# Kernel tuning notes

Measured on AMD Instinct MI355X. Metric: run time of the kernel, lower is better.

## Reference

```python
import jax, jax.numpy as jnp
import numpy as np

B, T, D, H = 2, 2048, 1024, 16

def setup_inputs() -> dict:
    key = jax.random.key(0)
    k0, k1, k2, k3 = jax.random.split(key, 4)
    s = 0.02
    return {
        "x": jax.random.normal(k0, (B, T, D), dtype=jnp.float32),
        "Wqkv": jax.random.normal(k1, (3 * D, D), dtype=jnp.float32) * s,
        "Wout": jax.random.normal(k2, (D, D), dtype=jnp.float32) * s,
        "bout": jax.random.normal(k3, (D,), dtype=jnp.float32) * s,
    }

def reference(x, Wqkv, Wout, bout):
    b, t, d = x.shape
    h = H
    dh = d // h
    qkv = x @ Wqkv.T  # [b,t,3d]
    q, k, v = jnp.split(qkv, 3, axis=-1)
    def merge_heads(z):
        return z.reshape(b, t, h, dh).transpose(0, 2, 1, 3)  # [b,h,t,dh]
    q, k, v = map(merge_heads, (q, k, v))
    scale = dh ** -0.5
    dots = jnp.einsum('bhid,bhjd->bhij', q, k) * scale  # [b,h,t,t]
    causal_mask = jnp.triu(jnp.ones((t, t), dtype=bool), 1)
    dots = jnp.where(causal_mask, -jnp.inf, dots)
    attn = jax.nn.softmax(dots, axis=-1)
    out = jnp.einsum('bhij,bhjd->bhid', attn, v)  # [b,h,t,dh]
    out = out.transpose(0, 2, 1, 3).reshape(b, t, d)
    return out @ Wout.T + bout
```

## Files before the change

kernel.cpp:

```cpp
#include <hip/hip_runtime.h>
#include <hip/hip_bf16.h>
#include <math.h>

typedef __bf16 bf16x8 __attribute__((ext_vector_type(8)));
typedef float f32x4 __attribute__((ext_vector_type(4)));
typedef unsigned short u16;
typedef unsigned int u32;

#define EXP2F(x) __builtin_amdgcn_exp2f(x)

constexpr int Bz = 2, T = 2048, D = 1024, H = 16;
constexpr int M = Bz * T;
constexpr int NQKV = 3 * D;
constexpr float SCALE2 = 0.125f * 1.44269504089f;

#define GLD_LDS16(g, l) __builtin_amdgcn_global_load_lds( \
    (__attribute__((address_space(1))) void*)(g),          \
    (__attribute__((address_space(3))) void*)(l), 16, 0, 0)

__global__ void f32_to_bf16_kernel(const float* __restrict__ in,
                                   u16* __restrict__ out, int n4) {
  int i = blockIdx.x * blockDim.x + threadIdx.x;
  int stride = gridDim.x * blockDim.x;
  for (; i < n4; i += stride) {
    float4 f = ((const float4*)in)[i];
    ushort4 u;
    u.x = __builtin_bit_cast(u16, (__bf16)f.x);
    u.y = __builtin_bit_cast(u16, (__bf16)f.y);
    u.z = __builtin_bit_cast(u16, (__bf16)f.z);
    u.w = __builtin_bit_cast(u16, (__bf16)f.w);
    ((ushort4*)out)[i] = u;
  }
}

template <bool FP32OUT, bool QSCALE>
__global__ __launch_bounds__(256, 2)
void gemm_bt(const u16* __restrict__ A, const u16* __restrict__ Bm,
             u16* __restrict__ outb, float* __restrict__ outf,
             const float* __restrict__ bias, int K, int ldc) {
  __shared__ __align__(16) u16 sA[128 * 64];
  __shared__ __align__(16) u16 sB[128 * 64];
  const int tid = threadIdx.x;
  const int lane = tid & 63;
  const int wid = tid >> 6;
  const int wr = wid >> 1, wc = wid & 1;

  const int nwg = gridDim.x * gridDim.y;
  const int flat = blockIdx.y * gridDim.x + blockIdx.x;
  const int cpx = nwg >> 3;
  const int swz = (flat & 7) * cpx + (flat >> 3);
  const int bx = swz % gridDim.x;
  const int by = swz / gridDim.x;

  const int row0 = by * 128;
  const int col0 = bx * 128;

  f32x4 acc[4][4];
#pragma unroll
  for (int m = 0; m < 4; ++m)
#pragma unroll
    for (int n = 0; n < 4; ++n) acc[m][n] = (f32x4){0.f, 0.f, 0.f, 0.f};

  const int nk = K >> 6;
  for (int kt = 0; kt < nk; ++kt) {
    const int k0 = kt << 6;
#pragma unroll
    for (int i = 0; i < 4; ++i) {
      int off = i * 4096 + tid * 16;
      int r = off >> 7;
      int cs = (off >> 4) & 7;
      int c = cs ^ (r & 7);
      const u16* ga = A + (size_t)(row0 + r) * K + k0 + c * 8;
      const u16* gb = Bm + (size_t)(col0 + r) * K + k0 + c * 8;
      u16* la = sA + (i * 4096 + (tid & ~63) * 16) / 2;
      u16* lb = sB + (i * 4096 + (tid & ~63) * 16) / 2;
      GLD_LDS16(ga, la);
      GLD_LDS16(gb, lb);
    }
    __syncthreads();
#pragma unroll
    for (int kk = 0; kk < 2; ++kk) {
      bf16x8 af[4], bfv[4];
#pragma unroll
      for (int m = 0; m < 4; ++m) {
        int r = wr * 64 + m * 16 + (lane & 15);
        int cs = (kk * 4 + (lane >> 4)) ^ (r & 7);
        af[m] = *(const bf16x8*)(sA + r * 64 + cs * 8);
      }
#pragma unroll
      for (int n = 0; n < 4; ++n) {
        int r = wc * 64 + n * 16 + (lane & 15);
        int cs = (kk * 4 + (lane >> 4)) ^ (r & 7);
        bfv[n] = *(const bf16x8*)(sB + r * 64 + cs * 8);
      }
#pragma unroll
      for (int m = 0; m < 4; ++m)
#pragma unroll
        for (int n = 0; n < 4; ++n)
          acc[m][n] = __builtin_amdgcn_mfma_f32_16x16x32_bf16(
              af[m], bfv[n], acc[m][n], 0, 0, 0);
    }
    __syncthreads();
  }

  const int orow0 = row0 + wr * 64;
  const int ocol0 = col0 + wc * 64;
#pragma unroll
  for (int m = 0; m < 4; ++m)
#pragma unroll
    for (int n = 0; n < 4; ++n)
#pragma unroll
      for (int j = 0; j < 4; ++j) {
        int rr = orow0 + m * 16 + (lane >> 4) * 4 + j;
        int cc = ocol0 + n * 16 + (lane & 15);
        if (FP32OUT) {
          outf[(size_t)rr * ldc + cc] = acc[m][n][j] + bias[cc];
        } else {
          float v = acc[m][n][j];
          if (QSCALE && cc < D) v *= SCALE2;
          outb[(size_t)rr * ldc + cc] = __builtin_bit_cast(u16, (__bf16)v);
        }
      }
}

__global__ __launch_bounds__(256, 3)
void flash_kernel(const u16* __restrict__ qkv, u16* __restrict__ attn_out) {
  __shared__ __align__(16) u16 sK[2][64 * 64];
  __shared__ __align__(16) u16 sVt[2][64 * 72];
  __shared__ __align__(16) u16 sP[4][16][72];

  const int tid = threadIdx.x;
  const int lane = tid & 63;
  const int l15 = lane & 15;
  const int hi = lane >> 4;
  const int w = tid >> 6;
  const int bh = blockIdx.x;
  const int b = bh >> 4, h = bh & 15;
  const int qt = (gridDim.y - 1) - blockIdx.y;
  const int q0 = qt * 64;
  const int nv = qt + 1;

  const size_t base = (size_t)b * T * 3072;
  const u16* qp = qkv + base + 0 * 1024 + h * 64;
  const u16* kp = qkv + base + 1 * 1024 + h * 64;
  const u16* vp = qkv + base + 2 * 1024 + h * 64;

  ushort4 vr[2][2];
  auto stageK = [&](u16* dst, int kt) {
#pragma unroll
    for (int i = 0; i < 2; ++i) {
      int off = i * 4096 + tid * 16;
      int r = off >> 7;
      int cs = (off >> 4) & 7;
      int c = cs ^ (r & 7);
      GLD_LDS16(kp + (size_t)(kt * 64 + r) * 3072 + c * 8,
                dst + (i * 4096 + (tid & ~63) * 16) / 2);
    }
  };
  auto loadV = [&](int kt) {
#pragma unroll
    for (int i = 0; i < 2; ++i) {
      const u16* gsrc = vp + (size_t)(kt * 64 + lane) * 3072 + (i * 4 + w) * 8;
      vr[i][0] = ((const ushort4*)gsrc)[0];
      vr[i][1] = ((const ushort4*)gsrc)[1];
    }
  };
  auto writeV = [&](u16* dst) {
#pragma unroll
    for (int i = 0; i < 2; ++i) {
      int c = i * 4 + w;
      dst[(c * 8 + 0) * 72 + lane] = vr[i][0].x;
      dst[(c * 8 + 1) * 72 + lane] = vr[i][0].y;
      dst[(c * 8 + 2) * 72 + lane] = vr[i][0].z;
      dst[(c * 8 + 3) * 72 + lane] = vr[i][0].w;
      dst[(c * 8 + 4) * 72 + lane] = vr[i][1].x;
      dst[(c * 8 + 5) * 72 + lane] = vr[i][1].y;
      dst[(c * 8 + 6) * 72 + lane] = vr[i][1].z;
      dst[(c * 8 + 7) * 72 + lane] = vr[i][1].w;
    }
  };

  bf16x8 qf[2];
#pragma unroll
  for (int kk = 0; kk < 2; ++kk)
    qf[kk] = *(const bf16x8*)(qp + (size_t)(q0 + w * 16 + l15) * 3072 +
                              kk * 32 + hi * 8);

  f32x4 o_acc[4];
#pragma unroll
  for (int n = 0; n < 4; ++n) o_acc[n] = (f32x4){0.f, 0.f, 0.f, 0.f};
  float m2 = -INFINITY, l_run = 0.f;

  stageK(sK[0], 0);
  loadV(0);
  writeV(sVt[0]);
  __syncthreads();

  for (int v = 0; v < nv; ++v) {
    const int cur = v & 1;
    const int k0 = v * 64;
    if (v + 1 < nv) {
      stageK(sK[cur ^ 1], v + 1);
      loadV(v + 1);
    }

    bf16x8 kf[2][4];
#pragma unroll
    for (int kk = 0; kk < 2; ++kk)
#pragma unroll
      for (int n = 0; n < 4; ++n) {
        int rk = n * 16 + l15;
        int cs = (kk * 4 + hi) ^ (rk & 7);
        kf[kk][n] = *(const bf16x8*)(&sK[cur][rk * 64 + cs * 8]);
      }

    f32x4 sc[4];
#pragma unroll
    for (int n = 0; n < 4; ++n) sc[n] = (f32x4){0.f, 0.f, 0.f, 0.f};
#pragma unroll
    for (int kk = 0; kk < 2; ++kk)
#pragma unroll
      for (int n = 0; n < 4; ++n)
        sc[n] = __builtin_amdgcn_mfma_f32_16x16x32_bf16(kf[kk][n], qf[kk],
                                                        sc[n], 0, 0, 0);

    const bool diag = (v == nv - 1);
    const int qrow = q0 + w * 16 + l15;
    float mx = -INFINITY;
#pragma unroll
    for (int n = 0; n < 4; ++n)
#pragma unroll
      for (int r = 0; r < 4; ++r) {
        float sv = sc[n][r];
        if (diag) {
          int kpos = k0 + n * 16 + hi * 4 + r;
          if (kpos > qrow) sv = -INFINITY;
        }
        sc[n][r] = sv;
        mx = fmaxf(mx, sv);
      }
    mx = fmaxf(mx, __shfl_xor(mx, 16, 64));
    mx = fmaxf(mx, __shfl_xor(mx, 32, 64));

    const bool skip = __all(mx <= m2);
    float alpha = 1.f;
    if (!skip) {
      float mn = fmaxf(m2, mx);
      alpha = EXP2F(m2 - mn);
      m2 = mn;
    }

    float sum = 0.f;
#pragma unroll
    for (int n = 0; n < 4; ++n) {
      float p0 = EXP2F(sc[n][0] - m2);
      float p1 = EXP2F(sc[n][1] - m2);
      float p2 = EXP2F(sc[n][2] - m2);
      float p3 = EXP2F(sc[n][3] - m2);
      sum += (p0 + p1) + (p2 + p3);
      u32 w01 = ((u32)__builtin_bit_cast(u16, (__bf16)p1) << 16) |
                __builtin_bit_cast(u16, (__bf16)p0);
      u32 w23 = ((u32)__builtin_bit_cast(u16, (__bf16)p3) << 16) |
                __builtin_bit_cast(u16, (__bf16)p2);
      *(u32*)(&sP[w][l15][n * 16 + hi * 4 + 0]) = w01;
      *(u32*)(&sP[w][l15][n * 16 + hi * 4 + 2]) = w23;
    }
    sum += __shfl_xor(sum, 16, 64);
    sum += __shfl_xor(sum, 32, 64);
    l_run = l_run * alpha + sum;

    bf16x8 vf[2][4];
#pragma unroll
    for (int ks = 0; ks < 2; ++ks)
#pragma unroll
      for (int n = 0; n < 4; ++n)
        vf[ks][n] = *(const bf16x8*)(
            &sVt[cur][(n * 16 + l15) * 72 + ks * 32 + hi * 8]);

    if (!skip) {
      float ab[4];
#pragma unroll
      for (int j = 0; j < 4; ++j) ab[j] = __shfl(alpha, hi * 4 + j, 64);
#pragma unroll
      for (int n = 0; n < 4; ++n)
#pragma unroll
        for (int j = 0; j < 4; ++j) o_acc[n][j] *= ab[j];
    }
#pragma unroll
    for (int ks = 0; ks < 2; ++ks) {
      bf16x8 pf = *(const bf16x8*)(&sP[w][l15][ks * 32 + hi * 8]);
#pragma unroll
      for (int n = 0; n < 4; ++n)
        o_acc[n] = __builtin_amdgcn_mfma_f32_16x16x32_bf16(pf, vf[ks][n],
                                                           o_acc[n], 0, 0, 0);
    }

    if (v + 1 < nv) {
      writeV(sVt[cur ^ 1]);
      __syncthreads();
    }
  }

#pragma unroll
  for (int j = 0; j < 4; ++j) {
    float lj = __shfl(l_run, hi * 4 + j, 64);
    float inv = 1.f / lj;
    int row = q0 + w * 16 + hi * 4 + j;
#pragma unroll
    for (int n = 0; n < 4; ++n) {
      int cc = h * 64 + n * 16 + l15;
      attn_out[((size_t)b * T + row) * 1024 + cc] =
          __builtin_bit_cast(u16, (__bf16)(o_acc[n][j] * inv));
    }
  }
}

extern "C" void kernel_launch(void* const* d_in, const int* in_sizes, int n_in,
                              void* d_out, int out_size, void* d_ws,
                              size_t ws_size, hipStream_t stream) {
  (void)in_sizes; (void)n_in; (void)out_size; (void)ws_size;
  const float* x = (const float*)d_in[0];
  const float* Wqkv = (const float*)d_in[1];
  const float* Wout = (const float*)d_in[2];
  const float* bout = (const float*)d_in[3];
  float* out = (float*)d_out;

  char* ws = (char*)d_ws;
  u16* x_bf = (u16*)(ws + 0);
  u16* wqkv_bf = (u16*)(ws + 8388608);
  u16* wout_bf = (u16*)(ws + 14680064);
  u16* qkvb = (u16*)(ws + 16777216);
  u16* aout = (u16*)(ws + 41943040);

  f32_to_bf16_kernel<<<2048, 256, 0, stream>>>(x, x_bf, M * D / 4);
  f32_to_bf16_kernel<<<2048, 256, 0, stream>>>(Wqkv, wqkv_bf, NQKV * D / 4);
  f32_to_bf16_kernel<<<1024, 256, 0, stream>>>(Wout, wout_bf, D * D / 4);

  gemm_bt<false, true><<<dim3(NQKV / 128, M / 128), 256, 0, stream>>>(
      x_bf, wqkv_bf, qkvb, nullptr, nullptr, D, NQKV);

  flash_kernel<<<dim3(Bz * H, T / 64), 256, 0, stream>>>(qkvb, aout);

  gemm_bt<true, false><<<dim3(D / 128, M / 128), 256, 0, stream>>>(
      aout, wout_bf, nullptr, out, bout, D, D);
}
```

Baseline: 113.4 us.

## Single-buffer flash attention K/V tiles for higher occupancy; fuse fp32-to-bf16 casts

The flash attention kernel drops double-buffered K and V^T shared-memory tiles for single buffers and raises the launch bound from 3 to 6 blocks per CU. K staging now happens after an extra barrier at the end of each iteration, so K loads no longer overlap compute; only V's global loads still prefetch into registers. Separately, the three fp32-to-bf16 conversion launches are merged into one kernel to remove launch overhead. The trade is more resident waves and less LDS per block against lost K prefetch overlap, an extra sync per tile, and possible register pressure from the tighter launch bound.

Result: slower. 123.2 us (+8.6%).

```diff
diff --git a/kernel.cpp b/kernel.cpp
--- a/kernel.cpp
+++ b/kernel.cpp
@@ -18,18 +18,31 @@
     (__attribute__((address_space(1))) void*)(g),          \
     (__attribute__((address_space(3))) void*)(l), 16, 0, 0)
 
-__global__ void f32_to_bf16_kernel(const float* __restrict__ in,
-                                   u16* __restrict__ out, int n4) {
+__global__ void cvt_all_kernel(const float* __restrict__ x,
+                               const float* __restrict__ wq,
+                               const float* __restrict__ wo,
+                               u16* __restrict__ xb, u16* __restrict__ wqb,
+                               u16* __restrict__ wob) {
+  constexpr int NX = M * D / 4;
+  constexpr int NQ = NQKV * D / 4;
+  constexpr int NW = D * D / 4;
+  constexpr int TOT = NX + NQ + NW;
   int i = blockIdx.x * blockDim.x + threadIdx.x;
   int stride = gridDim.x * blockDim.x;
-  for (; i < n4; i += stride) {
-    float4 f = ((const float4*)in)[i];
+  for (; i < TOT; i += stride) {
+    const float4* src;
+    u16* dst;
+    int j;
+    if (i < NX) { src = (const float4*)x; dst = xb; j = i; }
+    else if (i < NX + NQ) { src = (const float4*)wq; dst = wqb; j = i - NX; }
+    else { src = (const float4*)wo; dst = wob; j = i - NX - NQ; }
+    float4 f = src[j];
     ushort4 u;
     u.x = __builtin_bit_cast(u16, (__bf16)f.x);
     u.y = __builtin_bit_cast(u16, (__bf16)f.y);
     u.z = __builtin_bit_cast(u16, (__bf16)f.z);
     u.w = __builtin_bit_cast(u16, (__bf16)f.w);
-    ((ushort4*)out)[i] = u;
+    ((ushort4*)dst)[j] = u;
   }
 }
 
@@ -123,10 +136,10 @@
       }
 }
 
-__global__ __launch_bounds__(256, 3)
+__global__ __launch_bounds__(256, 6)
 void flash_kernel(const u16* __restrict__ qkv, u16* __restrict__ attn_out) {
-  __shared__ __align__(16) u16 sK[2][64 * 64];
-  __shared__ __align__(16) u16 sVt[2][64 * 72];
+  __shared__ __align__(16) u16 sK[64 * 64];
+  __shared__ __align__(16) u16 sVt[64 * 72];
   __shared__ __align__(16) u16 sP[4][16][72];
 
   const int tid = threadIdx.x;
@@ -146,7 +159,7 @@
   const u16* vp = qkv + base + 2 * 1024 + h * 64;
 
   ushort4 vr[2][2];
-  auto stageK = [&](u16* dst, int kt) {
+  auto stageK = [&](int kt) {
 #pragma unroll
     for (int i = 0; i < 2; ++i) {
       int off = i * 4096 + tid * 16;
@@ -154,7 +167,7 @@
       int cs = (off >> 4) & 7;
       int c = cs ^ (r & 7);
       GLD_LDS16(kp + (size_t)(kt * 64 + r) * 3072 + c * 8,
-                dst + (i * 4096 + (tid & ~63) * 16) / 2);
+                sK + (i * 4096 + (tid & ~63) * 16) / 2);
     }
   };
   auto loadV = [&](int kt) {
@@ -165,18 +178,18 @@
       vr[i][1] = ((const ushort4*)gsrc)[1];
     }
   };
-  auto writeV = [&](u16* dst) {
+  auto writeV = [&]() {
 #pragma unroll
     for (int i = 0; i < 2; ++i) {
       int c = i * 4 + w;
-      dst[(c * 8 + 0) * 72 + lane] = vr[i][0].x;
-      dst[(c * 8 + 1) * 72 + lane] = vr[i][0].y;
-      dst[(c * 8 + 2) * 72 + lane] = vr[i][0].z;
-      dst[(c * 8 + 3) * 72 + lane] = vr[i][0].w;
-      dst[(c * 8 + 4) * 72 + lane] = vr[i][1].x;
-      dst[(c * 8 + 5) * 72 + lane] = vr[i][1].y;
-      dst[(c * 8 + 6) * 72 + lane] = vr[i][1].z;
-      dst[(c * 8 + 7) * 72 + lane] = vr[i][1].w;
+      sVt[(c * 8 + 0) * 72 + lane] = vr[i][0].x;
+      sVt[(c * 8 + 1) * 72 + lane] = vr[i][0].y;
+      sVt[(c * 8 + 2) * 72 + lane] = vr[i][0].z;
+      sVt[(c * 8 + 3) * 72 + lane] = vr[i][0].w;
+      sVt[(c * 8 + 4) * 72 + lane] = vr[i][1].x;
+      sVt[(c * 8 + 5) * 72 + lane] = vr[i][1].y;
+      sVt[(c * 8 + 6) * 72 + lane] = vr[i][1].z;
+      sVt[(c * 8 + 7) * 72 + lane] = vr[i][1].w;
     }
   };
 
@@ -191,18 +204,14 @@
   for (int n = 0; n < 4; ++n) o_acc[n] = (f32x4){0.f, 0.f, 0.f, 0.f};
   float m2 = -INFINITY, l_run = 0.f;
 
-  stageK(sK[0], 0);
+  stageK(0);
   loadV(0);
-  writeV(sVt[0]);
+  writeV();
   __syncthreads();
 
   for (int v = 0; v < nv; ++v) {
-    const int cur = v & 1;
     const int k0 = v * 64;
-    if (v + 1 < nv) {
-      stageK(sK[cur ^ 1], v + 1);
-      loadV(v + 1);
-    }
+    if (v + 1 < nv) loadV(v + 1);
 
     bf16x8 kf[2][4];
 #pragma unroll
@@ -211,7 +220,7 @@
       for (int n = 0; n < 4; ++n) {
         int rk = n * 16 + l15;
         int cs = (kk * 4 + hi) ^ (rk & 7);
-        kf[kk][n] = *(const bf16x8*)(&sK[cur][rk * 64 + cs * 8]);
+        kf[kk][n] = *(const bf16x8*)(&sK[rk * 64 + cs * 8]);
       }
 
     f32x4 sc[4];
@@ -275,7 +284,7 @@
 #pragma unroll
       for (int n = 0; n < 4; ++n)
         vf[ks][n] = *(const bf16x8*)(
-            &sVt[cur][(n * 16 + l15) * 72 + ks * 32 + hi * 8]);
+            &sVt[(n * 16 + l15) * 72 + ks * 32 + hi * 8]);
 
     if (!skip) {
       float ab[4];
@@ -296,7 +305,9 @@
     }
 
     if (v + 1 < nv) {
-      writeV(sVt[cur ^ 1]);
+      __syncthreads();
+      stageK(v + 1);
+      writeV();
       __syncthreads();
     }
   }
@@ -332,9 +343,8 @@
   u16* qkvb = (u16*)(ws + 16777216);
   u16* aout = (u16*)(ws + 41943040);
 
-  f32_to_bf16_kernel<<<2048, 256, 0, stream>>>(x, x_bf, M * D / 4);
-  f32_to_bf16_kernel<<<2048, 256, 0, stream>>>(Wqkv, wqkv_bf, NQKV * D / 4);
-  f32_to_bf16_kernel<<<1024, 256, 0, stream>>>(Wout, wout_bf, D * D / 4);
+  cvt_all_kernel<<<2048, 256, 0, stream>>>(x, Wqkv, Wout, x_bf, wqkv_bf,
+                                           wout_bf);
 
   gemm_bt<false, true><<<dim3(NQKV / 128, M / 128), 256, 0, stream>>>(
       x_bf, wqkv_bf, qkvb, nullptr, nullptr, D, NQKV);
```
